# Performance work log

Hardware: AMD Instinct MI355X
Metric: run time of the kernel (lower is better)

Reference implementation:

```python
import jax, jax.numpy as jnp
import numpy as np

B, T, C, H, W = 2, 8, 256, 24, 24
NH = 8
HC = C // NH          # 32 head channels
KT, KHW = 3, 9        # offset conv kernel
ST, SHW = 2, 8        # offset conv stride
EPS = 1e-5


def _p(key, shape):
    return jax.random.normal(key, shape, dtype=jnp.float32) * 0.05


def setup_inputs() -> dict:
    ks = jax.random.split(jax.random.key(0), 16)
    return {
        "x": jax.random.normal(ks[0], (B, T, C, H, W), dtype=jnp.float32),
        "w_in": _p(ks[1], (C, C)), "b_in": _p(ks[2], (C,)),
        "w_q": _p(ks[3], (C, C)), "b_q": _p(ks[4], (C,)),
        "w_off_dw": _p(ks[5], (HC, 1, KT, KHW, KHW)), "b_off_dw": _p(ks[6], (HC,)),
        "ln_g": jnp.ones((HC,), jnp.float32), "ln_b": jnp.zeros((HC,), jnp.float32),
        "w_off_proj": _p(ks[7], (3, HC)),
        "w_k": _p(ks[8], (C, C)), "b_k": _p(ks[9], (C,)),
        "w_v": _p(ks[10], (C, C)), "b_v": _p(ks[11], (C,)),
        "rpe_w1": _p(ks[12], (32, 3)), "rpe_b1": _p(ks[13], (32,)),
        "rpe_w2": _p(ks[14], (1, 32)),
    }


def _conv1x1(x, w, b):
    # x: (B,C,T,H,W), w: (Co,Ci) -> pointwise Conv3d
    return jnp.einsum('bcthw,oc->bothw', x, w) + b[None, :, None, None, None]


def _trilinear(img, gx, gy, gz):
    # torch F.grid_sample(mode='bilinear', align_corners=True) for 5D input.
    # img: (G,Ch,T,H,W); gx->W axis, gy->H axis, gz->T axis, coords in [-1,1], shape (G,S)
    G, Ch, Td, Hd, Wd = img.shape
    ix = (gx + 1.0) * 0.5 * (Wd - 1)
    iy = (gy + 1.0) * 0.5 * (Hd - 1)
    iz = (gz + 1.0) * 0.5 * (Td - 1)
    x0 = jnp.floor(ix); y0 = jnp.floor(iy); z0 = jnp.floor(iz)
    fx = ix - x0; fy = iy - y0; fz = iz - z0
    x0i = jnp.clip(x0.astype(jnp.int32), 0, Wd - 1); x1i = jnp.clip(x0i + 1, 0, Wd - 1)
    y0i = jnp.clip(y0.astype(jnp.int32), 0, Hd - 1); y1i = jnp.clip(y0i + 1, 0, Hd - 1)
    z0i = jnp.clip(z0.astype(jnp.int32), 0, Td - 1); z1i = jnp.clip(z0i + 1, 0, Td - 1)
    bidx = jnp.arange(G)[:, None]

    def g(zi, yi, xi):
        return img[bidx, :, zi, yi, xi]  # (G,S,Ch)

    wz0, wz1 = (1.0 - fz)[..., None], fz[..., None]
    wy0, wy1 = (1.0 - fy)[..., None], fy[..., None]
    wx0, wx1 = (1.0 - fx)[..., None], fx[..., None]
    return (g(z0i, y0i, x0i) * wz0 * wy0 * wx0 + g(z0i, y0i, x1i) * wz0 * wy0 * wx1 +
            g(z0i, y1i, x0i) * wz0 * wy1 * wx0 + g(z0i, y1i, x1i) * wz0 * wy1 * wx1 +
            g(z1i, y0i, x0i) * wz1 * wy0 * wx0 + g(z1i, y0i, x1i) * wz1 * wy0 * wx1 +
            g(z1i, y1i, x0i) * wz1 * wy1 * wx0 + g(z1i, y1i, x1i) * wz1 * wy1 * wx1)


def reference(x, w_in, b_in, w_q, b_q, w_off_dw, b_off_dw, ln_g, ln_b, w_off_proj,
              w_k, b_k, w_v, b_v, rpe_w1, rpe_b1, rpe_w2):
    scale = HC ** (-0.5)
    xc = _conv1x1(jnp.transpose(x, (0, 2, 1, 3, 4)), w_in, b_in)       # (B,C,T,H,W)
    q = _conv1x1(xc, w_q, b_q)
    q_off = q.reshape(B * NH, HC, T, H, W)
    # depthwise offset conv: kernel (3,9,9), stride (2,8,8), pad (1,4,4)
    off = jax.lax.conv_general_dilated(
        q_off, w_off_dw, (ST, SHW, SHW),
        ((KT // 2, KT // 2), (KHW // 2, KHW // 2), (KHW // 2, KHW // 2)),
        dimension_numbers=('NCDHW', 'OIDHW', 'NCDHW'), feature_group_count=HC)
    off = off + b_off_dw[None, :, None, None, None]
    Tk, Hk, Wk = off.shape[2], off.shape[3], off.shape[4]
    o = jnp.transpose(off, (0, 2, 3, 4, 1))                             # (G,Tk,Hk,Wk,HC)
    mu = o.mean(-1, keepdims=True)
    var = ((o - mu) ** 2).mean(-1, keepdims=True)
    o = (o - mu) / jnp.sqrt(var + EPS) * ln_g + ln_b
    o = jax.nn.gelu(o, approximate=False)
    offset = jnp.einsum('bthwc,pc->bthwp', o, w_off_proj)               # (G,Tk,Hk,Wk,3)
    # reference points (linspace(0.5, K-0.5, K) normalized by (K-1))
    rt = ((jnp.arange(Tk, dtype=jnp.float32) + 0.5) / (Tk - 1.0)) * 2.0 - 1.0
    ry = ((jnp.arange(Hk, dtype=jnp.float32) + 0.5) / (Hk - 1.0)) * 2.0 - 1.0
    rx = ((jnp.arange(Wk, dtype=jnp.float32) + 0.5) / (Wk - 1.0)) * 2.0 - 1.0
    ref = jnp.stack(jnp.meshgrid(rt, ry, rx, indexing='ij'), axis=-1)   # (Tk,Hk,Wk,3)
    pos = jnp.clip(offset + ref, -1.0, 1.0)                             # offset_range_factor < 0 path
    G = B * NH
    n = Tk * Hk * Wk
    m = T * H * W
    posf = pos.reshape(G, n, 3)                                         # (t, y, x)
    # torch passes grid = pos[..., (0,2,1)] -> grid (x_w, y_h, z_t) = (pos_t, pos_x, pos_y)
    xs = _trilinear(xc.reshape(G, HC, T, H, W), posf[..., 0], posf[..., 2], posf[..., 1])  # (G,n,HC)
    x_sampled = jnp.transpose(xs, (0, 2, 1)).reshape(B, C, Tk, Hk, Wk)
    k = _conv1x1(x_sampled, w_k, b_k).reshape(G, HC, n)
    v = _conv1x1(x_sampled, w_v, b_v).reshape(G, HC, n)
    qf = q.reshape(G, HC, m)
    attn = jnp.einsum('bcm,bcn->bmn', qf, k) * scale                    # (G,m,n)
    # log-CPB bias (source normalizes y by W-1 and x by H-1; faithful)
    qt = (jnp.arange(T, dtype=jnp.float32) / (T - 1.0)) * 2.0 - 1.0
    qy = (jnp.arange(H, dtype=jnp.float32) / (W - 1.0)) * 2.0 - 1.0
    qx = (jnp.arange(W, dtype=jnp.float32) / (H - 1.0)) * 2.0 - 1.0
    qg = jnp.stack(jnp.meshgrid(qt, qy, qx, indexing='ij'), axis=-1).reshape(m, 3)
    disp = (qg[None, :, None, :] - posf[:, None, :, :]) * 4.0           # (G,m,n,3)
    disp = jnp.sign(disp) * jnp.log2(jnp.abs(disp) + 1.0) / 3.0         # log2(8) = 3
    hbias = jax.nn.relu(jnp.einsum('gmnp,hp->gmnh', disp, rpe_w1) + rpe_b1)
    attn = attn + jnp.einsum('gmnh,oh->gmno', hbias, rpe_w2)[..., 0]
    attn = jax.nn.softmax(attn, axis=2)
    out = jnp.einsum('bmn,bcn->bcm', attn, v).reshape(B, C, T, H, W)
    return jnp.transpose(out, (0, 2, 1, 3, 4))                          # (B,T,C,H,W)
```

## Files before the change

kernel.cpp:

```cpp
#include <hip/hip_runtime.h>
#include <hip/hip_bf16.h>

typedef unsigned short ushortT;
typedef __attribute__((ext_vector_type(8))) short bf16x8;
typedef __attribute__((ext_vector_type(4))) float f32x4;

#define WS_XC   0
#define WS_QB   2359296
#define WS_POS  3538944
#define WS_K    3540736
#define WS_V    3559168
#define WS_WC   3577600
#define WS_B512 3675904

__device__ __forceinline__ float bf2f(ushortT u) {
  union { unsigned int i; float f; } c; c.i = ((unsigned int)u) << 16; return c.f;
}
__device__ __forceinline__ ushortT f2bf(float f) {
  union { float f; unsigned int i; } c; c.f = f;
  unsigned int lsb = (c.i >> 16) & 1;
  return (ushortT)((c.i + 0x7fff + lsb) >> 16);
}
__device__ __forceinline__ float ldg_f(const void* p, int i, int bf) {
  return bf ? bf2f(((const ushortT*)p)[i]) : ((const float*)p)[i];
}
__device__ __forceinline__ int detect_bf(const void* x) {
  const ushortT* u = (const ushortT*)x;
  int wild = 0;
#pragma unroll
  for (int i = 0; i < 32; i++) {
    int e = (u[i] >> 7) & 0xFF;
    wild += (e != 0 && (e < 90 || e > 160)) ? 1 : 0;
  }
  return wild <= 4;
}

__global__ __launch_bounds__(256) void k_wc(const void* x, const void* w_in, const void* b_in,
                                            const void* w_q, const void* b_q,
                                            float* wc, float* bias512) {
  int o = blockIdx.x, tid = threadIdx.x;
  int bf = detect_bf(x);
  __shared__ float wq_s[256];
  __shared__ float red[256];
  wq_s[tid] = ldg_f(w_q, o * 256 + tid, bf);
  __syncthreads();
  float s = 0.f;
#pragma unroll 8
  for (int j = 0; j < 256; j++) s += wq_s[j] * ldg_f(w_in, j * 256 + tid, bf);
  wc[o * 256 + tid] = s;
  red[tid] = wq_s[tid] * ldg_f(b_in, tid, bf);
  __syncthreads();
  for (int m = 128; m; m >>= 1) {
    if (tid < m) red[tid] += red[tid + m];
    __syncthreads();
  }
  if (tid == 0) bias512[256 + o] = red[0] + ldg_f(b_q, o, bf);
  if (o == 0) bias512[tid] = ldg_f(b_in, tid, bf);
}

__global__ __launch_bounds__(256) void k_gemm_mfma(const void* x, const void* w_in, const float* wc,
                                                   const float* bias512, float* xc, ushortT* qb) {
  const int bf = detect_bf(x);
  __shared__ ushortT Ah[2][64 * 40], Al[2][64 * 40];
  __shared__ ushortT Bh[2][64 * 40], Bl[2][64 * 40];
  int tid = threadIdx.x;
  int bid = blockIdx.x;
  int colT = bid / 144, rowT = bid % 144;
  int col0 = colT * 64;
  int row0 = rowT * 64;
  int bt = row0 / 576;
  int hw0 = row0 % 576;
  const int isW = (col0 < 256);
  const ushortT* xB = (const ushortT*)x;
  const float*   xF = (const float*)x;
  const ushortT* wB = (const ushortT*)w_in;
  const float*   wF = (const float*)w_in;
  int ar = tid & 63, aoct = tid >> 6;
  int bn = tid >> 2, bko = tid & 3;
  int w = tid >> 6, l = tid & 63;
  int wr = w >> 1, wcq = w & 1;
  int lr = l & 15, lk = l >> 4;
  f32x4 acc[2][2] = {};

  float va[8], vb[8];
  auto loadA = [&](int kt) {
    int kbase = (bt * 256 + kt * 32 + aoct * 8) * 576 + hw0 + ar;
#pragma unroll
    for (int j = 0; j < 8; j++)
      va[j] = bf ? bf2f(xB[kbase + j * 576]) : xF[kbase + j * 576];
  };
  auto loadB = [&](int kt) {
    if (isW) {
      if (bf) {
        const ushortT* pp = wB + (col0 + bn) * 256 + kt * 32 + bko * 8;
#pragma unroll
        for (int j = 0; j < 8; j++) vb[j] = bf2f(pp[j]);
      } else {
        const float* pp = wF + (col0 + bn) * 256 + kt * 32 + bko * 8;
        float4 f0 = *(const float4*)pp;
        float4 f1 = *(const float4*)(pp + 4);
        vb[0] = f0.x; vb[1] = f0.y; vb[2] = f0.z; vb[3] = f0.w;
        vb[4] = f1.x; vb[5] = f1.y; vb[6] = f1.z; vb[7] = f1.w;
      }
    } else {
      const float* pp = wc + (col0 - 256 + bn) * 256 + kt * 32 + bko * 8;
      float4 f0 = *(const float4*)pp;
      float4 f1 = *(const float4*)(pp + 4);
      vb[0] = f0.x; vb[1] = f0.y; vb[2] = f0.z; vb[3] = f0.w;
      vb[4] = f1.x; vb[5] = f1.y; vb[6] = f1.z; vb[7] = f1.w;
    }
  };
  auto writeAB = [&](int buf) {
    ushortT hi[8], lo[8];
#pragma unroll
    for (int j = 0; j < 8; j++) {
      hi[j] = f2bf(va[j]);
      lo[j] = f2bf(va[j] - bf2f(hi[j]));
    }
    int4 ph, pl;
    ph.x = (int)((unsigned)hi[0] | ((unsigned)hi[1] << 16));
    ph.y = (int)((unsigned)hi[2] | ((unsigned)hi[3] << 16));
    ph.z = (int)((unsigned)hi[4] | ((unsigned)hi[5] << 16));
    ph.w = (int)((unsigned)hi[6] | ((unsigned)hi[7] << 16));
    pl.x = (int)((unsigned)lo[0] | ((unsigned)lo[1] << 16));
    pl.y = (int)((unsigned)lo[2] | ((unsigned)lo[3] << 16));
    pl.z = (int)((unsigned)lo[4] | ((unsigned)lo[5] << 16));
    pl.w = (int)((unsigned)lo[6] | ((unsigned)lo[7] << 16));
    *(int4*)&Ah[buf][ar * 40 + aoct * 8] = ph;
    *(int4*)&Al[buf][ar * 40 + aoct * 8] = pl;
#pragma unroll
    for (int j = 0; j < 8; j++) {
      hi[j] = f2bf(vb[j]);
      lo[j] = f2bf(vb[j] - bf2f(hi[j]));
    }
    ph.x = (int)((unsigned)hi[0] | ((unsigned)hi[1] << 16));
    ph.y = (int)((unsigned)hi[2] | ((unsigned)hi[3] << 16));
    ph.z = (int)((unsigned)hi[4] | ((unsigned)hi[5] << 16));
    ph.w = (int)((unsigned)hi[6] | ((unsigned)hi[7] << 16));
    pl.x = (int)((unsigned)lo[0] | ((unsigned)lo[1] << 16));
    pl.y = (int)((unsigned)lo[2] | ((unsigned)lo[3] << 16));
    pl.z = (int)((unsigned)lo[4] | ((unsigned)lo[5] << 16));
    pl.w = (int)((unsigned)lo[6] | ((unsigned)lo[7] << 16));
    *(int4*)&Bh[buf][bn * 40 + bko * 8] = ph;
    *(int4*)&Bl[buf][bn * 40 + bko * 8] = pl;
  };

  loadA(0); loadB(0);
  writeAB(0);
  __syncthreads();
  for (int kt = 0; kt < 8; kt++) {
    int cur = kt & 1;
    if (kt < 7) { loadA(kt + 1); loadB(kt + 1); }
    bf16x8 a0h = *(const bf16x8*)&Ah[cur][(wr * 32 + 0 * 16 + lr) * 40 + lk * 8];
    bf16x8 a1h = *(const bf16x8*)&Ah[cur][(wr * 32 + 1 * 16 + lr) * 40 + lk * 8];
    bf16x8 a0l = *(const bf16x8*)&Al[cur][(wr * 32 + 0 * 16 + lr) * 40 + lk * 8];
    bf16x8 a1l = *(const bf16x8*)&Al[cur][(wr * 32 + 1 * 16 + lr) * 40 + lk * 8];
    bf16x8 b0h = *(const bf16x8*)&Bh[cur][(wcq * 32 + 0 * 16 + lr) * 40 + lk * 8];
    bf16x8 b1h = *(const bf16x8*)&Bh[cur][(wcq * 32 + 1 * 16 + lr) * 40 + lk * 8];
    bf16x8 b0l = *(const bf16x8*)&Bl[cur][(wcq * 32 + 0 * 16 + lr) * 40 + lk * 8];
    bf16x8 b1l = *(const bf16x8*)&Bl[cur][(wcq * 32 + 1 * 16 + lr) * 40 + lk * 8];
    acc[0][0] = __builtin_amdgcn_mfma_f32_16x16x32_bf16(a0h, b0h, acc[0][0], 0, 0, 0);
    acc[0][0] = __builtin_amdgcn_mfma_f32_16x16x32_bf16(a0h, b0l, acc[0][0], 0, 0, 0);
    acc[0][0] = __builtin_amdgcn_mfma_f32_16x16x32_bf16(a0l, b0h, acc[0][0], 0, 0, 0);
    acc[0][1] = __builtin_amdgcn_mfma_f32_16x16x32_bf16(a0h, b1h, acc[0][1], 0, 0, 0);
    acc[0][1] = __builtin_amdgcn_mfma_f32_16x16x32_bf16(a0h, b1l, acc[0][1], 0, 0, 0);
    acc[0][1] = __builtin_amdgcn_mfma_f32_16x16x32_bf16(a0l, b1h, acc[0][1], 0, 0, 0);
    acc[1][0] = __builtin_amdgcn_mfma_f32_16x16x32_bf16(a1h, b0h, acc[1][0], 0, 0, 0);
    acc[1][0] = __builtin_amdgcn_mfma_f32_16x16x32_bf16(a1h, b0l, acc[1][0], 0, 0, 0);
    acc[1][0] = __builtin_amdgcn_mfma_f32_16x16x32_bf16(a1l, b0h, acc[1][0], 0, 0, 0);
    acc[1][1] = __builtin_amdgcn_mfma_f32_16x16x32_bf16(a1h, b1h, acc[1][1], 0, 0, 0);
    acc[1][1] = __builtin_amdgcn_mfma_f32_16x16x32_bf16(a1h, b1l, acc[1][1], 0, 0, 0);
    acc[1][1] = __builtin_amdgcn_mfma_f32_16x16x32_bf16(a1l, b1h, acc[1][1], 0, 0, 0);
    if (kt < 7) writeAB(cur ^ 1);
    __syncthreads();
  }
#pragma unroll
  for (int m = 0; m < 2; m++) {
#pragma unroll
    for (int n = 0; n < 2; n++) {
#pragma unroll
      for (int i = 0; i < 4; i++) {
        int row = row0 + wr * 32 + m * 16 + lk * 4 + i;
        int col = col0 + wcq * 32 + n * 16 + lr;
        float v = acc[m][n][i] + bias512[col];
        if (isW) xc[row * 256 + col] = v;
        else     qb[row * 256 + (col - 256)] = f2bf(v);
      }
    }
  }
}

__global__ __launch_bounds__(256) void k_offsets(const void* x, const ushortT* qb, const void* w_dw,
                                                 const void* b_dw, const void* ln_g, const void* ln_b,
                                                 const void* w_proj, float* pos) {
  __shared__ float wdw[243 * 33];
  __shared__ float part[8][33];
  int bid = blockIdx.x;
  int g = bid / 36, nn = bid % 36;
  int b = g >> 3, nh = g & 7;
  int tk = nn / 9, hk = (nn / 3) % 3, wk = nn % 3;
  int tid = threadIdx.x;
  int ch = tid & 31, grp = tid >> 5;
  int bf = detect_bf(x);
  for (int i = tid; i < 7776; i += 256) {
    int c = i / 243, tap = i % 243;
    wdw[tap * 33 + c] = ldg_f(w_dw, i, bf);
  }
  __syncthreads();
  float sum = 0.f;
  for (int tap = grp; tap < 243; tap += 8) {
    int dt = tap / 81, rem = tap % 81, dh = rem / 9, dw = rem % 9;
    int t = tk * 2 - 1 + dt, h = hk * 8 - 4 + dh, w = wk * 8 - 4 + dw;
    if (t < 0 || t >= 8 || h < 0 || h >= 24 || w < 0 || w >= 24) continue;
    float qv = bf2f(qb[((b * 8 + t) * 576 + h * 24 + w) * 256 + nh * 32 + ch]);
    sum += qv * wdw[tap * 33 + ch];
  }
  part[grp][ch] = sum;
  __syncthreads();
  if (tid < 32) {
    float v = ldg_f(b_dw, ch, bf);
#pragma unroll
    for (int j = 0; j < 8; j++) v += part[j][ch];
    float s1 = v;
    for (int m = 16; m; m >>= 1) s1 += __shfl_xor(s1, m);
    float mu = s1 * (1.f / 32.f);
    float d = v - mu;
    float s2 = d * d;
    for (int m = 16; m; m >>= 1) s2 += __shfl_xor(s2, m);
    float o = d * rsqrtf(s2 * (1.f / 32.f) + 1e-5f) * ldg_f(ln_g, ch, bf) + ldg_f(ln_b, ch, bf);
    o = 0.5f * o * (1.f + erff(o * 0.70710678118654752f));
    float res[3];
#pragma unroll
    for (int p = 0; p < 3; p++) {
      float t3 = o * ldg_f(w_proj, p * 32 + ch, bf);
      for (int m = 16; m; m >>= 1) t3 += __shfl_xor(t3, m);
      res[p] = t3;
    }
    if (ch == 0) {
      float ref0 = ((tk + 0.5f) / 3.f) * 2.f - 1.f;
      float ref1 = ((hk + 0.5f) / 2.f) * 2.f - 1.f;
      float ref2 = ((wk + 0.5f) / 2.f) * 2.f - 1.f;
      pos[bid * 3 + 0] = fminf(1.f, fmaxf(-1.f, res[0] + ref0));
      pos[bid * 3 + 1] = fminf(1.f, fmaxf(-1.f, res[1] + ref1));
      pos[bid * 3 + 2] = fminf(1.f, fmaxf(-1.f, res[2] + ref2));
    }
  }
}

__global__ __launch_bounds__(256) void k_svkv(const void* x, const float* xc_rm, const float* pos,
                                              const void* w_k, const void* b_k,
                                              const void* w_v, const void* b_v,
                                              float* k_rm, float* v_rm) {
  int bx = blockIdx.x;
  int sel = bx & 1, row = bx >> 1;
  int b = row / 36, nn = row % 36;
  int tid = threadIdx.x;
  int bf = detect_bf(x);
  __shared__ float a[256];
  {
    int nh = tid >> 5;
    int g = b * 8 + nh;
    float p0 = pos[(g * 36 + nn) * 3 + 0];
    float p1 = pos[(g * 36 + nn) * 3 + 1];
    float p2 = pos[(g * 36 + nn) * 3 + 2];
    float ix = (p0 + 1.f) * 0.5f * 23.f;
    float iy = (p2 + 1.f) * 0.5f * 23.f;
    float iz = (p1 + 1.f) * 0.5f * 7.f;
    float x0f = floorf(ix), y0f = floorf(iy), z0f = floorf(iz);
    float fx = ix - x0f, fy = iy - y0f, fz = iz - z0f;
    int x0 = min(max((int)x0f, 0), 23), x1 = min(x0 + 1, 23);
    int y0 = min(max((int)y0f, 0), 23), y1 = min(y0 + 1, 23);
    int z0 = min(max((int)z0f, 0), 7),  z1 = min(z0 + 1, 7);
#define AT(z, y, x) xc_rm[(((b * 8 + (z)) * 576 + (y) * 24 + (x)) * 256 + tid)]
    a[tid] =
      AT(z0, y0, x0) * (1.f - fz) * (1.f - fy) * (1.f - fx) + AT(z0, y0, x1) * (1.f - fz) * (1.f - fy) * fx +
      AT(z0, y1, x0) * (1.f - fz) * fy * (1.f - fx)         + AT(z0, y1, x1) * (1.f - fz) * fy * fx +
      AT(z1, y0, x0) * fz * (1.f - fy) * (1.f - fx)         + AT(z1, y0, x1) * fz * (1.f - fy) * fx +
      AT(z1, y1, x0) * fz * fy * (1.f - fx)                 + AT(z1, y1, x1) * fz * fy * fx;
#undef AT
  }
  __syncthreads();
  const void* w = sel ? w_v : w_k;
  const void* bb = sel ? b_v : b_k;
  float s = 0.f;
  if (bf) {
    const ushortT* wp = (const ushortT*)w + tid * 256;
#pragma unroll 4
    for (int c = 0; c < 256; c += 8) {
      ushort4 k0 = *(const ushort4*)(wp + c), k1 = *(const ushort4*)(wp + c + 4);
      s += a[c+0]*bf2f(k0.x) + a[c+1]*bf2f(k0.y) + a[c+2]*bf2f(k0.z) + a[c+3]*bf2f(k0.w)
         + a[c+4]*bf2f(k1.x) + a[c+5]*bf2f(k1.y) + a[c+6]*bf2f(k1.z) + a[c+7]*bf2f(k1.w);
    }
  } else {
    const float* wp = (const float*)w + tid * 256;
#pragma unroll 4
    for (int c = 0; c < 256; c += 4) {
      float4 k4 = *(const float4*)(wp + c);
      s += a[c]*k4.x + a[c+1]*k4.y + a[c+2]*k4.z + a[c+3]*k4.w;
    }
  }
  float* outp = sel ? v_rm : k_rm;
  outp[row * 256 + tid] = s + ldg_f(bb, tid, bf);
}

__global__ __launch_bounds__(256) void k_attn(const void* x, const ushortT* qb, const float* k_rm,
                                              const float* v_rm, const float* pos, const void* rpe_w1,
                                              const void* rpe_b1, const void* rpe_w2, void* outp) {
  __shared__ float ks[36][32];
  __shared__ float vs[36][32];
  __shared__ float poss[36][4];
  __shared__ float4 wab[32];
  __shared__ float w2s[32];
  int g = blockIdx.y, b = g >> 3, nh = g & 7;
  int tid = threadIdx.x;
  int bf = detect_bf(x);
  for (int e = tid; e < 36 * 32; e += 256) {
    int nn = e >> 5, ch = e & 31;
    ks[nn][ch] = k_rm[(b * 36 + nn) * 256 + nh * 32 + ch];
    vs[nn][ch] = v_rm[(b * 36 + nn) * 256 + nh * 32 + ch];
  }
  if (tid < 32) {
    wab[tid] = make_float4(ldg_f(rpe_w1, tid * 3 + 0, bf), ldg_f(rpe_w1, tid * 3 + 1, bf),
                           ldg_f(rpe_w1, tid * 3 + 2, bf), ldg_f(rpe_b1, tid, bf));
    w2s[tid] = ldg_f(rpe_w2, tid, bf);
  }
  if (tid < 108) poss[tid / 3][tid % 3] = pos[g * 108 + tid];
  __syncthreads();

  int mm = blockIdx.x * 256 + tid;
  int t = mm / 576, hw = mm % 576, hh = hw / 24, wwi = hw % 24;
  float qreg[32];
  const ushort4* qp = (const ushort4*)&qb[(b * 4608 + mm) * 256 + nh * 32];
#pragma unroll
  for (int i = 0; i < 8; i++) {
    ushort4 u = qp[i];
    qreg[i * 4 + 0] = bf2f(u.x); qreg[i * 4 + 1] = bf2f(u.y);
    qreg[i * 4 + 2] = bf2f(u.z); qreg[i * 4 + 3] = bf2f(u.w);
  }
  float qg0 = t * (2.f / 7.f) - 1.f;
  float qg1 = hh * (2.f / 23.f) - 1.f;
  float qg2 = wwi * (2.f / 23.f) - 1.f;
  const float scale = 0.17677669529663687f;
  float p[36];
  float mx = -1e30f;
#pragma unroll
  for (int nn = 0; nn < 36; nn++) {
    float s = 0.f;
#pragma unroll
    for (int ch = 0; ch < 32; ch++) s += qreg[ch] * ks[nn][ch];
    float d0 = (qg0 - poss[nn][0]) * 4.f;
    float d1 = (qg1 - poss[nn][1]) * 4.f;
    float d2 = (qg2 - poss[nn][2]) * 4.f;
    d0 = copysignf(__log2f(fabsf(d0) + 1.f) * (1.f / 3.f), d0);
    d1 = copysignf(__log2f(fabsf(d1) + 1.f) * (1.f / 3.f), d1);
    d2 = copysignf(__log2f(fabsf(d2) + 1.f) * (1.f / 3.f), d2);
    float bias = 0.f;
#pragma unroll
    for (int h = 0; h < 32; h++) {
      float4 w = wab[h];
      float hb = fmaf(d0, w.x, fmaf(d1, w.y, fmaf(d2, w.z, w.w)));
      bias = fmaf(fmaxf(hb, 0.f), w2s[h], bias);
    }
    float L = fmaf(s, scale, bias);
    p[nn] = L;
    mx = fmaxf(mx, L);
  }
  float se = 0.f;
#pragma unroll
  for (int nn = 0; nn < 36; nn++) {
    float e = __expf(p[nn] - mx);
    p[nn] = e;
    se += e;
  }
  float inv = 1.f / se;
  float acc[32] = {};
#pragma unroll
  for (int nn = 0; nn < 36; nn++) {
    float pr = p[nn] * inv;
#pragma unroll
    for (int ch = 0; ch < 32; ch++) acc[ch] += pr * vs[nn][ch];
  }
  int obase = ((b * 8 + t) * 256 + nh * 32) * 576 + hw;
  if (bf) {
    __hip_bfloat16* o = (__hip_bfloat16*)outp;
#pragma unroll
    for (int ch = 0; ch < 32; ch++) o[obase + ch * 576] = __float2bfloat16(acc[ch]);
  } else {
    float* o = (float*)outp;
#pragma unroll
    for (int ch = 0; ch < 32; ch++) o[obase + ch * 576] = acc[ch];
  }
}

extern "C" void kernel_launch(void* const* d_in, const int* in_sizes, int n_in,
                              void* d_out, int out_size, void* d_ws, size_t ws_size,
                              hipStream_t stream) {
  const void* x        = d_in[0];
  const void* w_in     = d_in[1];
  const void* b_in     = d_in[2];
  const void* w_q      = d_in[3];
  const void* b_q      = d_in[4];
  const void* w_off_dw = d_in[5];
  const void* b_off_dw = d_in[6];
  const void* ln_g     = d_in[7];
  const void* ln_b     = d_in[8];
  const void* w_off_pj = d_in[9];
  const void* w_k      = d_in[10];
  const void* b_k      = d_in[11];
  const void* w_v      = d_in[12];
  const void* b_v      = d_in[13];
  const void* rpe_w1   = d_in[14];
  const void* rpe_b1   = d_in[15];
  const void* rpe_w2   = d_in[16];

  float* ws    = (float*)d_ws;
  float* xc    = ws + WS_XC;
  ushortT* qb  = (ushortT*)(ws + WS_QB);
  float* pos   = ws + WS_POS;
  float* krm   = ws + WS_K;
  float* vrm   = ws + WS_V;
  float* wcf   = ws + WS_WC;
  float* b512  = ws + WS_B512;

  k_wc<<<256, 256, 0, stream>>>(x, w_in, b_in, w_q, b_q, wcf, b512);
  k_gemm_mfma<<<1152, 256, 0, stream>>>(x, w_in, wcf, b512, xc, qb);
  k_offsets<<<576, 256, 0, stream>>>(x, qb, w_off_dw, b_off_dw, ln_g, ln_b, w_off_pj, pos);
  k_svkv<<<144, 256, 0, stream>>>(x, xc, pos, w_k, b_k, w_v, b_v, krm, vrm);
  k_attn<<<dim3(18, 16), 256, 0, stream>>>(x, qb, krm, vrm, pos, rpe_w1, rpe_b1, rpe_w2, d_out);
}
```

Before: 120.5 us.

## Read attention K/V and RPE weights via scalar loads instead of LDS; truncating hi/lo split

```diff
diff --git a/kernel.cpp b/kernel.cpp
--- a/kernel.cpp
+++ b/kernel.cpp
@@ -111,36 +111,36 @@
     }
   };
   auto writeAB = [&](int buf) {
-    ushortT hi[8], lo[8];
+    unsigned ua[8], ra[8];
 #pragma unroll
     for (int j = 0; j < 8; j++) {
-      hi[j] = f2bf(va[j]);
-      lo[j] = f2bf(va[j] - bf2f(hi[j]));
+      ua[j] = __float_as_uint(va[j]);
+      ra[j] = __float_as_uint(va[j] - __uint_as_float(ua[j] & 0xffff0000u));
     }
     int4 ph, pl;
-    ph.x = (int)((unsigned)hi[0] | ((unsigned)hi[1] << 16));
-    ph.y = (int)((unsigned)hi[2] | ((unsigned)hi[3] << 16));
-    ph.z = (int)((unsigned)hi[4] | ((unsigned)hi[5] << 16));
-    ph.w = (int)((unsigned)hi[6] | ((unsigned)hi[7] << 16));
-    pl.x = (int)((unsigned)lo[0] | ((unsigned)lo[1] << 16));
-    pl.y = (int)((unsigned)lo[2] | ((unsigned)lo[3] << 16));
-    pl.z = (int)((unsigned)lo[4] | ((unsigned)lo[5] << 16));
-    pl.w = (int)((unsigned)lo[6] | ((unsigned)lo[7] << 16));
+    ph.x = (int)((ua[0] >> 16) | (ua[1] & 0xffff0000u));
+    ph.y = (int)((ua[2] >> 16) | (ua[3] & 0xffff0000u));
+    ph.z = (int)((ua[4] >> 16) | (ua[5] & 0xffff0000u));
+    ph.w = (int)((ua[6] >> 16) | (ua[7] & 0xffff0000u));
+    pl.x = (int)((ra[0] >> 16) | (ra[1] & 0xffff0000u));
+    pl.y = (int)((ra[2] >> 16) | (ra[3] & 0xffff0000u));
+    pl.z = (int)((ra[4] >> 16) | (ra[5] & 0xffff0000u));
+    pl.w = (int)((ra[6] >> 16) | (ra[7] & 0xffff0000u));
     *(int4*)&Ah[buf][ar * 40 + aoct * 8] = ph;
     *(int4*)&Al[buf][ar * 40 + aoct * 8] = pl;
 #pragma unroll
     for (int j = 0; j < 8; j++) {
-      hi[j] = f2bf(vb[j]);
-      lo[j] = f2bf(vb[j] - bf2f(hi[j]));
-    }
-    ph.x = (int)((unsigned)hi[0] | ((unsigned)hi[1] << 16));
-    ph.y = (int)((unsigned)hi[2] | ((unsigned)hi[3] << 16));
-    ph.z = (int)((unsigned)hi[4] | ((unsigned)hi[5] << 16));
-    ph.w = (int)((unsigned)hi[6] | ((unsigned)hi[7] << 16));
-    pl.x = (int)((unsigned)lo[0] | ((unsigned)lo[1] << 16));
-    pl.y = (int)((unsigned)lo[2] | ((unsigned)lo[3] << 16));
-    pl.z = (int)((unsigned)lo[4] | ((unsigned)lo[5] << 16));
-    pl.w = (int)((unsigned)lo[6] | ((unsigned)lo[7] << 16));
+      ua[j] = __float_as_uint(vb[j]);
+      ra[j] = __float_as_uint(vb[j] - __uint_as_float(ua[j] & 0xffff0000u));
+    }
+    ph.x = (int)((ua[0] >> 16) | (ua[1] & 0xffff0000u));
+    ph.y = (int)((ua[2] >> 16) | (ua[3] & 0xffff0000u));
+    ph.z = (int)((ua[4] >> 16) | (ua[5] & 0xffff0000u));
+    ph.w = (int)((ua[6] >> 16) | (ua[7] & 0xffff0000u));
+    pl.x = (int)((ra[0] >> 16) | (ra[1] & 0xffff0000u));
+    pl.y = (int)((ra[2] >> 16) | (ra[3] & 0xffff0000u));
+    pl.z = (int)((ra[4] >> 16) | (ra[5] & 0xffff0000u));
+    pl.w = (int)((ra[6] >> 16) | (ra[7] & 0xffff0000u));
     *(int4*)&Bh[buf][bn * 40 + bko * 8] = ph;
     *(int4*)&Bl[buf][bn * 40 + bko * 8] = pl;
   };
@@ -303,30 +303,15 @@
   outp[row * 256 + tid] = s + ldg_f(bb, tid, bf);
 }
 
-__global__ __launch_bounds__(256) void k_attn(const void* x, const ushortT* qb, const float* k_rm,
-                                              const float* v_rm, const float* pos, const void* rpe_w1,
-                                              const void* rpe_b1, const void* rpe_w2, void* outp) {
-  __shared__ float ks[36][32];
-  __shared__ float vs[36][32];
-  __shared__ float poss[36][4];
-  __shared__ float4 wab[32];
-  __shared__ float w2s[32];
+__global__ __launch_bounds__(256) void k_attn(const void* x, const ushortT* qb,
+                                              const float* __restrict__ k_rm,
+                                              const float* __restrict__ v_rm,
+                                              const float* __restrict__ pos,
+                                              const void* rpe_w1, const void* rpe_b1,
+                                              const void* rpe_w2, void* outp) {
   int g = blockIdx.y, b = g >> 3, nh = g & 7;
   int tid = threadIdx.x;
   int bf = detect_bf(x);
-  for (int e = tid; e < 36 * 32; e += 256) {
-    int nn = e >> 5, ch = e & 31;
-    ks[nn][ch] = k_rm[(b * 36 + nn) * 256 + nh * 32 + ch];
-    vs[nn][ch] = v_rm[(b * 36 + nn) * 256 + nh * 32 + ch];
-  }
-  if (tid < 32) {
-    wab[tid] = make_float4(ldg_f(rpe_w1, tid * 3 + 0, bf), ldg_f(rpe_w1, tid * 3 + 1, bf),
-                           ldg_f(rpe_w1, tid * 3 + 2, bf), ldg_f(rpe_b1, tid, bf));
-    w2s[tid] = ldg_f(rpe_w2, tid, bf);
-  }
-  if (tid < 108) poss[tid / 3][tid % 3] = pos[g * 108 + tid];
-  __syncthreads();
-
   int mm = blockIdx.x * 256 + tid;
   int t = mm / 576, hw = mm % 576, hh = hw / 24, wwi = hw % 24;
   float qreg[32];
@@ -337,34 +322,53 @@
     qreg[i * 4 + 0] = bf2f(u.x); qreg[i * 4 + 1] = bf2f(u.y);
     qreg[i * 4 + 2] = bf2f(u.z); qreg[i * 4 + 3] = bf2f(u.w);
   }
+  const float* __restrict__ kb = k_rm + (b * 36) * 256 + nh * 32;
+  const float* __restrict__ vb = v_rm + (b * 36) * 256 + nh * 32;
+  const float* __restrict__ pp = pos + g * 108;
   float qg0 = t * (2.f / 7.f) - 1.f;
   float qg1 = hh * (2.f / 23.f) - 1.f;
   float qg2 = wwi * (2.f / 23.f) - 1.f;
   const float scale = 0.17677669529663687f;
   float p[36];
-  float mx = -1e30f;
 #pragma unroll
   for (int nn = 0; nn < 36; nn++) {
     float s = 0.f;
 #pragma unroll
-    for (int ch = 0; ch < 32; ch++) s += qreg[ch] * ks[nn][ch];
-    float d0 = (qg0 - poss[nn][0]) * 4.f;
-    float d1 = (qg1 - poss[nn][1]) * 4.f;
-    float d2 = (qg2 - poss[nn][2]) * 4.f;
-    d0 = copysignf(__log2f(fabsf(d0) + 1.f) * (1.f / 3.f), d0);
-    d1 = copysignf(__log2f(fabsf(d1) + 1.f) * (1.f / 3.f), d1);
-    d2 = copysignf(__log2f(fabsf(d2) + 1.f) * (1.f / 3.f), d2);
-    float bias = 0.f;
-#pragma unroll
-    for (int h = 0; h < 32; h++) {
-      float4 w = wab[h];
-      float hb = fmaf(d0, w.x, fmaf(d1, w.y, fmaf(d2, w.z, w.w)));
-      bias = fmaf(fmaxf(hb, 0.f), w2s[h], bias);
-    }
-    float L = fmaf(s, scale, bias);
-    p[nn] = L;
-    mx = fmaxf(mx, L);
-  }
+    for (int ch = 0; ch < 32; ch++) s += qreg[ch] * kb[nn * 256 + ch];
+    p[nn] = s * scale;
+  }
+#pragma unroll
+  for (int hc = 0; hc < 4; hc++) {
+    float wx[8], wy[8], wz[8], wbb[8], w2[8];
+#pragma unroll
+    for (int j = 0; j < 8; j++) {
+      int h = hc * 8 + j;
+      wx[j]  = ldg_f(rpe_w1, h * 3 + 0, bf);
+      wy[j]  = ldg_f(rpe_w1, h * 3 + 1, bf);
+      wz[j]  = ldg_f(rpe_w1, h * 3 + 2, bf);
+      wbb[j] = ldg_f(rpe_b1, h, bf);
+      w2[j]  = ldg_f(rpe_w2, h, bf);
+    }
+#pragma unroll
+    for (int nn = 0; nn < 36; nn++) {
+      float d0 = (qg0 - pp[nn * 3 + 0]) * 4.f;
+      float d1 = (qg1 - pp[nn * 3 + 1]) * 4.f;
+      float d2 = (qg2 - pp[nn * 3 + 2]) * 4.f;
+      d0 = copysignf(__log2f(fabsf(d0) + 1.f) * (1.f / 3.f), d0);
+      d1 = copysignf(__log2f(fabsf(d1) + 1.f) * (1.f / 3.f), d1);
+      d2 = copysignf(__log2f(fabsf(d2) + 1.f) * (1.f / 3.f), d2);
+      float bias = 0.f;
+#pragma unroll
+      for (int j = 0; j < 8; j++) {
+        float hb = fmaf(d0, wx[j], fmaf(d1, wy[j], fmaf(d2, wz[j], wbb[j])));
+        bias = fmaf(fmaxf(hb, 0.f), w2[j], bias);
+      }
+      p[nn] += bias;
+    }
+  }
+  float mx = -1e30f;
+#pragma unroll
+  for (int nn = 0; nn < 36; nn++) mx = fmaxf(mx, p[nn]);
   float se = 0.f;
 #pragma unroll
   for (int nn = 0; nn < 36; nn++) {
@@ -378,7 +382,7 @@
   for (int nn = 0; nn < 36; nn++) {
     float pr = p[nn] * inv;
 #pragma unroll
-    for (int ch = 0; ch < 32; ch++) acc[ch] += pr * vs[nn][ch];
+    for (int ch = 0; ch < 32; ch++) acc[ch] += pr * vb[nn * 256 + ch];
   }
   int obase = ((b * 8 + t) * 256 + nh * 32) * 576 + hw;
   if (bf) {
```

Result: slower. 206.7 us (+71.5%).
